# Kernel optimization log

Measured on AMD Instinct MI355X. Metric: run time of the kernel, lower is better.

The kernel has to match this reference:

```python
import jax, jax.numpy as jnp
import numpy as np

N, E, IN_DIM, HID, G = 100000, 3200000, 128, 64, 256


def setup_inputs() -> dict:
    key = jax.random.key(0)
    ks = jax.random.split(key, 10)
    x = jax.random.normal(ks[0], (N, IN_DIM), dtype=jnp.float32)
    ei = jax.random.randint(ks[1], (2, E), 0, N, dtype=jnp.int64)
    ew = jax.random.uniform(ks[2], (E,), dtype=jnp.float32)
    batch = jnp.sort(jax.random.randint(ks[3], (N,), 0, G, dtype=jnp.int64))
    W1 = jax.random.normal(ks[4], (IN_DIM, HID), dtype=jnp.float32) * 0.05
    b1 = jnp.zeros((HID,), dtype=jnp.float32)
    W2 = jax.random.normal(ks[5], (HID, HID), dtype=jnp.float32) * 0.05
    b2 = jnp.zeros((HID,), dtype=jnp.float32)
    Wc = jax.random.normal(ks[6], (HID, 1), dtype=jnp.float32) * 0.05
    bc = jnp.zeros((1,), dtype=jnp.float32)
    return {"x": x, "ei": ei, "ew": ew, "batch": batch,
            "W1": W1, "b1": b1, "W2": W2, "b2": b2, "Wc": Wc, "bc": bc}


def _gcn_norm(ei, ew, n):
    # PyG gcn_norm: add self-loops (weight 1), symmetric deg^-1/2 normalization
    loop = jnp.arange(n, dtype=ei.dtype)
    row = jnp.concatenate([ei[0], loop])
    col = jnp.concatenate([ei[1], loop])
    w = jnp.concatenate([ew, jnp.ones((n,), dtype=ew.dtype)])
    deg = jax.ops.segment_sum(w, col, num_segments=n)
    dis = jnp.where(deg > 0, jax.lax.rsqrt(jnp.maximum(deg, 1e-30)), 0.0)
    norm = dis[row] * w * dis[col]
    return row, col, norm


def _gcn_conv(x, row, col, norm, W, b, n):
    xl = x @ W                                   # [N, hid]
    msg = xl[row] * norm[:, None]                # gather + scale, [E+N, hid]
    return jax.ops.segment_sum(msg, col, num_segments=n) + b


def reference(x, ei, ew, batch, W1, b1, W2, b2, Wc, bc):
    n = x.shape[0]
    row, col, norm = _gcn_norm(ei, ew, n)
    h = jax.nn.relu(_gcn_conv(x, row, col, norm, W1, b1, n))
    h = jax.nn.relu(_gcn_conv(h, row, col, norm, W2, b2, n))
    # global mean pool over graphs
    sums = jax.ops.segment_sum(h, batch, num_segments=G)           # [G, hid]
    cnt = jax.ops.segment_sum(jnp.ones((n,), h.dtype), batch, num_segments=G)
    pooled = sums / jnp.maximum(cnt, 1.0)[:, None]
    return (pooled @ Wc + bc).reshape(-1)                           # [G]
```

## Files before the change

kernel.cpp:

```cpp
#include <hip/hip_runtime.h>

#define N_NODES 100000
#define N_PAD   100352
#define N_EDGES 3200000
#define IN_DIM  128
#define HID     64
#define N_GRAPHS 256
#define NB      392
#define NBLK    256
#define EPB     (N_EDGES / NBLK)
#define G1ROWS  32
#define G1BLK   (N_NODES / G1ROWS)

typedef unsigned short ushort_t;
typedef unsigned int   uint_t;

__device__ __forceinline__ ushort_t f2bf(float v) {
    uint_t b = __float_as_uint(v);
    b += 0x7fffu + ((b >> 16) & 1u);
    return (ushort_t)(b >> 16);
}
__device__ __forceinline__ void bf2f2(uint_t u, float& lo, float& hi) {
    lo = __uint_as_float(u << 16);
    hi = __uint_as_float(u & 0xffff0000u);
}
__device__ __forceinline__ void ld_bf16x8(const ushort_t* p, float4& a, float4& b) {
    uint4 u = *(const uint4*)p;
    bf2f2(u.x, a.x, a.y); bf2f2(u.y, a.z, a.w);
    bf2f2(u.z, b.x, b.y); bf2f2(u.w, b.z, b.w);
}
__device__ __forceinline__ void fma8(float4& a0, float4& a1, const uint4& u, float w) {
    float lo, hi;
    bf2f2(u.x, lo, hi); a0.x += lo * w; a0.y += hi * w;
    bf2f2(u.y, lo, hi); a0.z += lo * w; a0.w += hi * w;
    bf2f2(u.z, lo, hi); a1.x += lo * w; a1.y += hi * w;
    bf2f2(u.w, lo, hi); a1.z += lo * w; a1.w += hi * w;
}
__device__ __forceinline__ int2 ldrec(const int2* __restrict__ csr, int last, int idx) {
    int2 r = csr[idx <= last ? idx : last];
    if (idx > last) r.y = 0;
    return r;
}

__global__ __launch_bounds__(256) void bhist_gemm1_kernel(
        const int* __restrict__ col, int* __restrict__ H,
        const float* __restrict__ x, const float* __restrict__ W1,
        ushort_t* __restrict__ xl) {
    __shared__ float sW[IN_DIM * HID];
    __shared__ float sx[G1ROWS][IN_DIM];
    int tid = threadIdx.x;
    if (blockIdx.x < NBLK) {
        int (*h)[NB] = (int (*)[NB])sW;
        for (int i = tid; i < NB; i += 256) { h[0][i] = 0; h[1][i] = 0; }
        __syncthreads();
        const int4* col4 = (const int4*)col;
        int base4 = blockIdx.x * (EPB / 4);
        int sel = tid & 1;
        for (int j = tid; j < EPB / 4; j += 256) {
            int4 c = col4[base4 + j];
            atomicAdd(&h[sel][c.x >> 8], 1);
            atomicAdd(&h[sel][c.y >> 8], 1);
            atomicAdd(&h[sel][c.z >> 8], 1);
            atomicAdd(&h[sel][c.w >> 8], 1);
        }
        __syncthreads();
        for (int i = tid; i < NB; i += 256) H[i * NBLK + blockIdx.x] = h[0][i] + h[1][i];
    } else {
        int bid = blockIdx.x - NBLK;
        const float4* W4  = (const float4*)W1;
        float4*       sW4 = (float4*)sW;
        #pragma unroll
        for (int i = 0; i < 8; ++i) sW4[tid + 256 * i] = W4[tid + 256 * i];
        int r0 = bid * G1ROWS;
        const float4* x4  = (const float4*)(x + (size_t)r0 * IN_DIM);
        float4*       sx4 = (float4*)&sx[0][0];
        #pragma unroll
        for (int i = 0; i < 4; ++i) sx4[tid + 256 * i] = x4[tid + 256 * i];
        __syncthreads();
        int c  = tid & 63;
        int rb = (tid >> 6) * 8;
        float acc0 = 0.f, acc1 = 0.f, acc2 = 0.f, acc3 = 0.f;
        float acc4 = 0.f, acc5 = 0.f, acc6 = 0.f, acc7 = 0.f;
        #pragma unroll 4
        for (int k4 = 0; k4 < IN_DIM; k4 += 4) {
            float4 x0 = *(const float4*)&sx[rb + 0][k4];
            float4 x1 = *(const float4*)&sx[rb + 1][k4];
            float4 x2 = *(const float4*)&sx[rb + 2][k4];
            float4 x3 = *(const float4*)&sx[rb + 3][k4];
            float4 x4r = *(const float4*)&sx[rb + 4][k4];
            float4 x5 = *(const float4*)&sx[rb + 5][k4];
            float4 x6 = *(const float4*)&sx[rb + 6][k4];
            float4 x7 = *(const float4*)&sx[rb + 7][k4];
            #pragma unroll
            for (int kk = 0; kk < 4; ++kk) {
                float wk = sW[(k4 + kk) * HID + c];
                acc0 += ((const float*)&x0)[kk] * wk;
                acc1 += ((const float*)&x1)[kk] * wk;
                acc2 += ((const float*)&x2)[kk] * wk;
                acc3 += ((const float*)&x3)[kk] * wk;
                acc4 += ((const float*)&x4r)[kk] * wk;
                acc5 += ((const float*)&x5)[kk] * wk;
                acc6 += ((const float*)&x6)[kk] * wk;
                acc7 += ((const float*)&x7)[kk] * wk;
            }
        }
        ushort_t* o = xl + (size_t)(r0 + rb) * HID + c;
        o[0 * HID] = f2bf(acc0);
        o[1 * HID] = f2bf(acc1);
        o[2 * HID] = f2bf(acc2);
        o[3 * HID] = f2bf(acc3);
        o[4 * HID] = f2bf(acc4);
        o[5 * HID] = f2bf(acc5);
        o[6 * HID] = f2bf(acc6);
        o[7 * HID] = f2bf(acc7);
    }
}

__global__ __launch_bounds__(256) void scan1_kernel(int* H, int* __restrict__ bsum) {
    __shared__ int s[256];
    int i = blockIdx.x * 256 + threadIdx.x;
    int v = H[i];
    s[threadIdx.x] = v;
    __syncthreads();
    #pragma unroll
    for (int off = 1; off < 256; off <<= 1) {
        int t = (threadIdx.x >= off) ? s[threadIdx.x - off] : 0;
        __syncthreads();
        s[threadIdx.x] += t;
        __syncthreads();
    }
    H[i] = s[threadIdx.x] - v;
    if (threadIdx.x == 255) bsum[blockIdx.x] = s[255];
}

__global__ __launch_bounds__(256) void bscatter_kernel(const int* __restrict__ row,
                                                       const int* __restrict__ col,
                                                       const float* __restrict__ ew,
                                                       const int* __restrict__ H,
                                                       const int* __restrict__ bsum,
                                                       int* __restrict__ boff,
                                                       int2* __restrict__ recs) {
    __shared__ int2 lrec[EPB];
    __shared__ int  lofs[NB];
    __shared__ int  hcnt[NB];
    __shared__ int  gofs[NB];
    __shared__ int  cur[NB];
    __shared__ int  s[256];
    __shared__ int  carry;
    int tid = threadIdx.x, blk = blockIdx.x;
    if (tid == 0) carry = 0;
    __syncthreads();
    for (int c = 0; c < 2; ++c) {
        int i = c * 256 + tid;
        int v = (i < NB) ? bsum[i] : 0;
        s[tid] = v;
        __syncthreads();
        #pragma unroll
        for (int off = 1; off < 256; off <<= 1) {
            int t = (tid >= off) ? s[tid - off] : 0;
            __syncthreads();
            s[tid] += t;
            __syncthreads();
        }
        if (i < NB) {
            int tb = s[tid] - v + carry;
            int ex = H[i * NBLK + blk];
            gofs[i] = tb + ex;
            hcnt[i] = ((blk < NBLK - 1) ? H[i * NBLK + blk + 1] : v) - ex;
            if (blk == 0) boff[i] = tb;
        }
        __syncthreads();
        if (tid == 0) carry += s[255];
        __syncthreads();
    }
    if (tid == 0) carry = 0;
    __syncthreads();
    for (int c = 0; c < 2; ++c) {
        int i = c * 256 + tid;
        int v = (i < NB) ? hcnt[i] : 0;
        s[tid] = v;
        __syncthreads();
        #pragma unroll
        for (int off = 1; off < 256; off <<= 1) {
            int t = (tid >= off) ? s[tid - off] : 0;
            __syncthreads();
            s[tid] += t;
            __syncthreads();
        }
        if (i < NB) { int l = s[tid] - v + carry; lofs[i] = l; cur[i] = l; }
        __syncthreads();
        if (tid == 0) carry += s[255];
        __syncthreads();
    }
    const int4*   row4 = (const int4*)row;
    const int4*   col4 = (const int4*)col;
    const float4* ew4  = (const float4*)ew;
    int base4 = blk * (EPB / 4);
    for (int j = tid; j < EPB / 4; j += 256) {
        int4   r4 = row4[base4 + j];
        int4   c4 = col4[base4 + j];
        float4 w4 = ew4[base4 + j];
        int p0 = atomicAdd(&cur[c4.x >> 8], 1);
        lrec[p0] = make_int2(r4.x | ((c4.x & 255) << 17), __float_as_int(w4.x));
        int p1 = atomicAdd(&cur[c4.y >> 8], 1);
        lrec[p1] = make_int2(r4.y | ((c4.y & 255) << 17), __float_as_int(w4.y));
        int p2 = atomicAdd(&cur[c4.z >> 8], 1);
        lrec[p2] = make_int2(r4.z | ((c4.z & 255) << 17), __float_as_int(w4.z));
        int p3 = atomicAdd(&cur[c4.w >> 8], 1);
        lrec[p3] = make_int2(r4.w | ((c4.w & 255) << 17), __float_as_int(w4.w));
    }
    __syncthreads();
    int wv = tid >> 6, lane = tid & 63;
    for (int i = wv; i < NB; i += 4) {
        int cnt = hcnt[i], lo = lofs[i], go = gofs[i];
        for (int k = lane; k < cnt; k += 64)
            recs[go + k] = lrec[lo + k];
    }
}

__global__ __launch_bounds__(256) void degcsr_kernel(const int2* __restrict__ recs,
                                                     const int* __restrict__ boff,
                                                     float* __restrict__ dis,
                                                     int* __restrict__ rowptr,
                                                     int2* __restrict__ csr,
                                                     ushort_t* xl) {
    __shared__ int   cnt[256];
    __shared__ float degf[256];
    __shared__ int   sscan[256];
    __shared__ int   cur[256];
    int b = blockIdx.x, tid = threadIdx.x;
    cnt[tid] = 0; degf[tid] = 0.f;
    __syncthreads();
    int s = boff[b], e = (b + 1 < NB) ? boff[b + 1] : N_EDGES;
    for (int j = s + tid; j < e; j += 256) {
        int2 r = recs[j];
        int cl = (r.x >> 17) & 255;
        atomicAdd(&cnt[cl], 1);
        atomicAdd(&degf[cl], __int_as_float(r.y));
    }
    __syncthreads();
    int c = cnt[tid];
    sscan[tid] = c;
    __syncthreads();
    #pragma unroll
    for (int off = 1; off < 256; off <<= 1) {
        int t = (tid >= off) ? sscan[tid - off] : 0;
        __syncthreads();
        sscan[tid] += t;
        __syncthreads();
    }
    int rp = s + sscan[tid] - c;
    rowptr[b * 256 + tid] = rp;
    cur[tid] = rp;
    float d = 1.0f / sqrtf(fmaxf(1.0f + degf[tid], 1e-30f));
    dis[b * 256 + tid] = d;
    __syncthreads();
    degf[tid] = d;
    __syncthreads();
    for (int j = s + tid; j < e; j += 256) {
        int2 r = recs[j];
        int cl = (r.x >> 17) & 255;
        int pos = atomicAdd(&cur[cl], 1);
        csr[pos] = r;
    }
    int n0 = b * 256;
    for (int i = tid; i < 256 * 8; i += 256) {
        int r = i >> 3;
        int n = n0 + r;
        if (n >= N_NODES) break;
        uint4* p = (uint4*)(xl + (size_t)n * HID) + (i & 7);
        float d2 = degf[r];
        uint4 u = *p;
        float lo, hi;
        uint_t w0, w1, w2, w3;
        bf2f2(u.x, lo, hi); w0 = f2bf(lo * d2) | ((uint_t)f2bf(hi * d2) << 16);
        bf2f2(u.y, lo, hi); w1 = f2bf(lo * d2) | ((uint_t)f2bf(hi * d2) << 16);
        bf2f2(u.z, lo, hi); w2 = f2bf(lo * d2) | ((uint_t)f2bf(hi * d2) << 16);
        bf2f2(u.w, lo, hi); w3 = f2bf(lo * d2) | ((uint_t)f2bf(hi * d2) << 16);
        *p = make_uint4(w0, w1, w2, w3);
    }
}

__device__ __forceinline__ void gather_row16(const int2* __restrict__ csr,
                                             const ushort_t* __restrict__ xl,
                                             int base, int end, int n,
                                             int g, int c0, int lane,
                                             float4& a0, float4& a1) {
    a0 = make_float4(0.f, 0.f, 0.f, 0.f);
    a1 = make_float4(0.f, 0.f, 0.f, 0.f);
    if (g == 0) {
        ld_bf16x8(xl + (uint_t)(n * HID + c0), a0, a1);
    }
    int tot  = end - base;
    int half = (tot + 1) >> 1;
    int gs   = base + (g ? half : 0);
    int m    = g ? (tot - half) : half;
    if (m > 0) {
        int last = gs + m - 1;
        int li4  = lane & 3;
        int gb   = lane & 56;
        int nb   = (m + 3) >> 2;

#define BCI(r_, u0_, u1_, u2_, u3_, w0_, w1_, w2_, w3_) do {                     \
        int r0_ = __shfl((r_).x, gb + 0, 64), r1_ = __shfl((r_).x, gb + 1, 64);  \
        int r2_ = __shfl((r_).x, gb + 2, 64), r3_ = __shfl((r_).x, gb + 3, 64);  \
        w0_ = __int_as_float(__shfl((r_).y, gb + 0, 64));                         \
        w1_ = __int_as_float(__shfl((r_).y, gb + 1, 64));                         \
        w2_ = __int_as_float(__shfl((r_).y, gb + 2, 64));                         \
        w3_ = __int_as_float(__shfl((r_).y, gb + 3, 64));                         \
        u0_ = *(const uint4*)(xl + (uint_t)((r0_ & 0x1FFFF) * HID + c0));         \
        u1_ = *(const uint4*)(xl + (uint_t)((r1_ & 0x1FFFF) * HID + c0));         \
        u2_ = *(const uint4*)(xl + (uint_t)((r2_ & 0x1FFFF) * HID + c0));         \
        u3_ = *(const uint4*)(xl + (uint_t)((r3_ & 0x1FFFF) * HID + c0));         \
    } while (0)

        uint4 uA0, uA1, uA2, uA3, uB0, uB1, uB2, uB3;
        float wA0, wA1, wA2, wA3, wB0, wB1, wB2, wB3;
        int2 rA = ldrec(csr, last, gs + li4);
        int2 rB = (nb > 1) ? ldrec(csr, last, gs + 4 + li4) : rA;
        BCI(rA, uA0, uA1, uA2, uA3, wA0, wA1, wA2, wA3);
        int blk = 0;
        while (true) {
            bool hasB  = (blk + 1 < nb);
            bool hasA2 = (blk + 2 < nb);
            if (hasA2) rA = ldrec(csr, last, gs + (blk + 2) * 4 + li4);
            if (hasB) { BCI(rB, uB0, uB1, uB2, uB3, wB0, wB1, wB2, wB3); }
            fma8(a0, a1, uA0, wA0); fma8(a0, a1, uA1, wA1);
            fma8(a0, a1, uA2, wA2); fma8(a0, a1, uA3, wA3);
            if (!hasB) break;
            bool hasB2 = (blk + 3 < nb);
            if (hasB2) rB = ldrec(csr, last, gs + (blk + 3) * 4 + li4);
            if (hasA2) { BCI(rA, uA0, uA1, uA2, uA3, wA0, wA1, wA2, wA3); }
            fma8(a0, a1, uB0, wB0); fma8(a0, a1, uB1, wB1);
            fma8(a0, a1, uB2, wB2); fma8(a0, a1, uB3, wB3);
            if (!hasA2) break;
            blk += 2;
        }
#undef BCI
    }
    a0.x += __shfl_down(a0.x, 8, 64); a0.y += __shfl_down(a0.y, 8, 64);
    a0.z += __shfl_down(a0.z, 8, 64); a0.w += __shfl_down(a0.w, 8, 64);
    a1.x += __shfl_down(a1.x, 8, 64); a1.y += __shfl_down(a1.y, 8, 64);
    a1.z += __shfl_down(a1.z, 8, 64); a1.w += __shfl_down(a1.w, 8, 64);
}

__global__ __launch_bounds__(256) void gather_gemm2_kernel(
        const int2* __restrict__ csr, const int* __restrict__ rowptr,
        const float* __restrict__ dis, const ushort_t* __restrict__ xl,
        const float* __restrict__ W2, const float* __restrict__ b1,
        ushort_t* __restrict__ xl2) {
    __shared__ float sW[HID * HID];
    __shared__ float sh[16][HID + 4];
    int tid = threadIdx.x;
    const float4* W4  = (const float4*)W2;
    float4*       sW4 = (float4*)sW;
    #pragma unroll
    for (int i = 0; i < 4; ++i) sW4[tid + 256 * i] = W4[tid + 256 * i];

    int n0   = blockIdx.x * 16;
    int wv   = tid >> 6;
    int lane = tid & 63;
    int lr   = wv * 4 + (lane >> 4);
    int n    = n0 + lr;
    int g    = (lane >> 3) & 1;
    int c0   = (lane & 7) << 3;
    int base = rowptr[n], end = rowptr[n + 1];
    float d  = dis[n];
    float4 a0, a1;
    gather_row16(csr, xl, base, end, n, g, c0, lane, a0, a1);
    if (g == 0) {
        float4 bb0 = *(const float4*)(b1 + c0);
        float4 bb1 = *(const float4*)(b1 + c0 + 4);
        float4 h0 = make_float4(fmaxf(a0.x * d + bb0.x, 0.f), fmaxf(a0.y * d + bb0.y, 0.f),
                                fmaxf(a0.z * d + bb0.z, 0.f), fmaxf(a0.w * d + bb0.w, 0.f));
        float4 h1 = make_float4(fmaxf(a1.x * d + bb1.x, 0.f), fmaxf(a1.y * d + bb1.y, 0.f),
                                fmaxf(a1.z * d + bb1.z, 0.f), fmaxf(a1.w * d + bb1.w, 0.f));
        *(float4*)(&sh[lr][c0])     = h0;
        *(float4*)(&sh[lr][c0 + 4]) = h1;
    }
    __syncthreads();
    int cc = tid & 63, rq = tid >> 6;
    float acc0 = 0.f, acc1 = 0.f, acc2 = 0.f, acc3 = 0.f;
    #pragma unroll 8
    for (int k = 0; k < HID; ++k) {
        float wk = sW[k * HID + cc];
        acc0 += sh[rq * 4 + 0][k] * wk;
        acc1 += sh[rq * 4 + 1][k] * wk;
        acc2 += sh[rq * 4 + 2][k] * wk;
        acc3 += sh[rq * 4 + 3][k] * wk;
    }
    xl2[(size_t)(n0 + rq * 4 + 0) * HID + cc] = f2bf(acc0 * dis[n0 + rq * 4 + 0]);
    xl2[(size_t)(n0 + rq * 4 + 1) * HID + cc] = f2bf(acc1 * dis[n0 + rq * 4 + 1]);
    xl2[(size_t)(n0 + rq * 4 + 2) * HID + cc] = f2bf(acc2 * dis[n0 + rq * 4 + 2]);
    xl2[(size_t)(n0 + rq * 4 + 3) * HID + cc] = f2bf(acc3 * dis[n0 + rq * 4 + 3]);
}

__global__ __launch_bounds__(256) void gather_pool_kernel(
        const int2* __restrict__ csr, const int* __restrict__ rowptr,
        const float* __restrict__ dis, const ushort_t* __restrict__ xl,
        const float* __restrict__ b2, const float* __restrict__ Wc,
        float* __restrict__ sval) {
    int tid  = threadIdx.x;
    int n    = (blockIdx.x * 256 + tid) >> 4;
    int lane = tid & 63;
    int g    = (lane >> 3) & 1;
    int c0   = (lane & 7) << 3;
    int base = rowptr[n], end = rowptr[n + 1];
    float d  = dis[n];
    float4 a0, a1;
    gather_row16(csr, xl, base, end, n, g, c0, lane, a0, a1);
    float4 bb0 = *(const float4*)(b2 + c0);
    float4 bb1 = *(const float4*)(b2 + c0 + 4);
    float4 wc0 = *(const float4*)(Wc + c0);
    float4 wc1 = *(const float4*)(Wc + c0 + 4);
    float s = fmaxf(a0.x * d + bb0.x, 0.f) * wc0.x + fmaxf(a0.y * d + bb0.y, 0.f) * wc0.y
            + fmaxf(a0.z * d + bb0.z, 0.f) * wc0.z + fmaxf(a0.w * d + bb0.w, 0.f) * wc0.w
            + fmaxf(a1.x * d + bb1.x, 0.f) * wc1.x + fmaxf(a1.y * d + bb1.y, 0.f) * wc1.y
            + fmaxf(a1.z * d + bb1.z, 0.f) * wc1.z + fmaxf(a1.w * d + bb1.w, 0.f) * wc1.w;
    s += __shfl_down(s, 4, 64);
    s += __shfl_down(s, 2, 64);
    s += __shfl_down(s, 1, 64);
    if ((lane & 15) == 0) sval[n] = s;
}

__global__ __launch_bounds__(256) void final_out_kernel(const float* __restrict__ sval,
                                                        const int* __restrict__ batch,
                                                        const float* __restrict__ bc,
                                                        float* __restrict__ out) {
    __shared__ float s[256];
    int g = blockIdx.x;
    int lo = 0, hi = N_NODES;
    while (lo < hi) { int m = (lo + hi) >> 1; if (batch[m] < g) lo = m + 1; else hi = m; }
    int start = lo;
    hi = N_NODES;
    while (lo < hi) { int m = (lo + hi) >> 1; if (batch[m] < g + 1) lo = m + 1; else hi = m; }
    int end = lo;
    float acc = 0.f;
    for (int i = start + threadIdx.x; i < end; i += 256) acc += sval[i];
    s[threadIdx.x] = acc;
    __syncthreads();
    #pragma unroll
    for (int off = 128; off > 0; off >>= 1) {
        if (threadIdx.x < off) s[threadIdx.x] += s[threadIdx.x + off];
        __syncthreads();
    }
    if (threadIdx.x == 0)
        out[g] = s[0] / fmaxf((float)(end - start), 1.0f) + bc[0];
}

extern "C" void kernel_launch(void* const* d_in, const int* in_sizes, int n_in,
                              void* d_out, int out_size, void* d_ws, size_t ws_size,
                              hipStream_t stream) {
    const float* x     = (const float*)d_in[0];
    const int*   ei    = (const int*)  d_in[1];
    const float* ew    = (const float*)d_in[2];
    const int*   batch = (const int*)  d_in[3];
    const float* W1    = (const float*)d_in[4];
    const float* b1    = (const float*)d_in[5];
    const float* W2    = (const float*)d_in[6];
    const float* b2    = (const float*)d_in[7];
    const float* Wc    = (const float*)d_in[8];
    const float* bc    = (const float*)d_in[9];
    float* out = (float*)d_out;

    const int* row = ei;
    const int* col = ei + N_EDGES;

    int2*     recs   = (int2*)d_ws;
    ushort_t* xlA    = (ushort_t*)(recs + N_EDGES);
    ushort_t* xlB    = xlA + (size_t)N_NODES * HID;
    int2*     csr    = (int2*)(xlB + (size_t)N_NODES * HID);
    int*      rowptr = (int*)(csr + N_EDGES);
    float*    dis    = (float*)(rowptr + N_PAD);
    int*      bsum   = (int*)(dis + N_PAD);
    int*      boff   = bsum + 512;
    float*    sval   = (float*)(boff + 512);
    int*      H      = (int*)csr;

    bhist_gemm1_kernel<<<NBLK + G1BLK, 256, 0, stream>>>(col, H, x, W1, xlA);
    scan1_kernel    <<<NB,   256, 0, stream>>>(H, bsum);
    bscatter_kernel <<<NBLK, 256, 0, stream>>>(row, col, ew, H, bsum, boff, recs);
    degcsr_kernel   <<<NB,   256, 0, stream>>>(recs, boff, dis, rowptr, csr, xlA);
    gather_gemm2_kernel<<<N_NODES / 16, 256, 0, stream>>>(csr, rowptr, dis, xlA, W2, b1, xlB);
    gather_pool_kernel <<<N_NODES / 16, 256, 0, stream>>>(csr, rowptr, dis, xlB, b2, Wc, sval);
    final_out_kernel<<<N_GRAPHS, 256, 0, stream>>>(sval, batch, bc, out);
}
```

Before: 360.5 us.

## Compute GEMM1 one row per thread with W1 read from global memory

Restructures the first GEMM so each thread computes a full 64-wide output row, holding 64 accumulators in registers. W1 is read through uniform global (cached) loads instead of being staged in shared memory, and the output is written as packed bf16 uint4 stores. This removes the 32 KB+16 KB shared-memory staging and the barrier, which should raise occupancy alongside the histogram blocks. In exchange, each thread reads its x row with strided, uncoalesced accesses, and the high register pressure may limit occupancy or cause spills.

```diff
diff --git a/kernel.cpp b/kernel.cpp
--- a/kernel.cpp
+++ b/kernel.cpp
@@ -9,8 +9,8 @@
 #define NB      392
 #define NBLK    256
 #define EPB     (N_EDGES / NBLK)
-#define G1ROWS  32
-#define G1BLK   (N_NODES / G1ROWS)
+#define G1ROWS  256
+#define G1BLK   ((N_NODES + G1ROWS - 1) / G1ROWS)
 
 typedef unsigned short ushort_t;
 typedef unsigned int   uint_t;
@@ -46,11 +46,9 @@
         const int* __restrict__ col, int* __restrict__ H,
         const float* __restrict__ x, const float* __restrict__ W1,
         ushort_t* __restrict__ xl) {
-    __shared__ float sW[IN_DIM * HID];
-    __shared__ float sx[G1ROWS][IN_DIM];
+    __shared__ int h[2][NB];
     int tid = threadIdx.x;
     if (blockIdx.x < NBLK) {
-        int (*h)[NB] = (int (*)[NB])sW;
         for (int i = tid; i < NB; i += 256) { h[0][i] = 0; h[1][i] = 0; }
         __syncthreads();
         const int4* col4 = (const int4*)col;
@@ -67,52 +65,39 @@
         for (int i = tid; i < NB; i += 256) H[i * NBLK + blockIdx.x] = h[0][i] + h[1][i];
     } else {
         int bid = blockIdx.x - NBLK;
-        const float4* W4  = (const float4*)W1;
-        float4*       sW4 = (float4*)sW;
+        int r   = bid * G1ROWS + tid;
+        if (r >= N_NODES) return;
+        float acc[HID];
         #pragma unroll
-        for (int i = 0; i < 8; ++i) sW4[tid + 256 * i] = W4[tid + 256 * i];
-        int r0 = bid * G1ROWS;
-        const float4* x4  = (const float4*)(x + (size_t)r0 * IN_DIM);
-        float4*       sx4 = (float4*)&sx[0][0];
-        #pragma unroll
-        for (int i = 0; i < 4; ++i) sx4[tid + 256 * i] = x4[tid + 256 * i];
-        __syncthreads();
-        int c  = tid & 63;
-        int rb = (tid >> 6) * 8;
-        float acc0 = 0.f, acc1 = 0.f, acc2 = 0.f, acc3 = 0.f;
-        float acc4 = 0.f, acc5 = 0.f, acc6 = 0.f, acc7 = 0.f;
-        #pragma unroll 4
-        for (int k4 = 0; k4 < IN_DIM; k4 += 4) {
-            float4 x0 = *(const float4*)&sx[rb + 0][k4];
-            float4 x1 = *(const float4*)&sx[rb + 1][k4];
-            float4 x2 = *(const float4*)&sx[rb + 2][k4];
-            float4 x3 = *(const float4*)&sx[rb + 3][k4];
-            float4 x4r = *(const float4*)&sx[rb + 4][k4];
-            float4 x5 = *(const float4*)&sx[rb + 5][k4];
-            float4 x6 = *(const float4*)&sx[rb + 6][k4];
-            float4 x7 = *(const float4*)&sx[rb + 7][k4];
+        for (int c = 0; c < HID; ++c) acc[c] = 0.f;
+        const float4* xr = (const float4*)(x + (size_t)r * IN_DIM);
+        const float4* w4 = (const float4*)W1;
+        for (int k4 = 0; k4 < IN_DIM / 4; ++k4) {
+            float4 xv = xr[k4];
             #pragma unroll
             for (int kk = 0; kk < 4; ++kk) {
-                float wk = sW[(k4 + kk) * HID + c];
-                acc0 += ((const float*)&x0)[kk] * wk;
-                acc1 += ((const float*)&x1)[kk] * wk;
-                acc2 += ((const float*)&x2)[kk] * wk;
-                acc3 += ((const float*)&x3)[kk] * wk;
-                acc4 += ((const float*)&x4r)[kk] * wk;
-                acc5 += ((const float*)&x5)[kk] * wk;
-                acc6 += ((const float*)&x6)[kk] * wk;
-                acc7 += ((const float*)&x7)[kk] * wk;
+                float xk = ((const float*)&xv)[kk];
+                const float4* wrow = w4 + (k4 * 4 + kk) * (HID / 4);
+                #pragma unroll
+                for (int c4 = 0; c4 < HID / 4; ++c4) {
+                    float4 wv = wrow[c4];
+                    acc[c4 * 4 + 0] += xk * wv.x;
+                    acc[c4 * 4 + 1] += xk * wv.y;
+                    acc[c4 * 4 + 2] += xk * wv.z;
+                    acc[c4 * 4 + 3] += xk * wv.w;
+                }
             }
         }
-        ushort_t* o = xl + (size_t)(r0 + rb) * HID + c;
-        o[0 * HID] = f2bf(acc0);
-        o[1 * HID] = f2bf(acc1);
-        o[2 * HID] = f2bf(acc2);
-        o[3 * HID] = f2bf(acc3);
-        o[4 * HID] = f2bf(acc4);
-        o[5 * HID] = f2bf(acc5);
-        o[6 * HID] = f2bf(acc6);
-        o[7 * HID] = f2bf(acc7);
+        uint4* o = (uint4*)(xl + (size_t)r * HID);
+        #pragma unroll
+        for (int j = 0; j < 8; ++j) {
+            uint4 u;
+            u.x = (uint_t)f2bf(acc[j * 8 + 0]) | ((uint_t)f2bf(acc[j * 8 + 1]) << 16);
+            u.y = (uint_t)f2bf(acc[j * 8 + 2]) | ((uint_t)f2bf(acc[j * 8 + 3]) << 16);
+            u.z = (uint_t)f2bf(acc[j * 8 + 4]) | ((uint_t)f2bf(acc[j * 8 + 5]) << 16);
+            u.w = (uint_t)f2bf(acc[j * 8 + 6]) | ((uint_t)f2bf(acc[j * 8 + 7]) << 16);
+            o[j] = u;
+        }
     }
 }
 
```

New measurement: 388.2 us. 1.08x slower.
